# Optimization experiments

Hardware: AMD Instinct MI355X
Metric: run time of the kernel (lower is better)

The kernel has to match this reference:

```python
import math
import jax, jax.numpy as jnp
import numpy as np

B, Q, K, D = 32, 1024, 1024, 128
MASK_VALUE = -1000000.0


def setup_inputs() -> dict:
    key = jax.random.key(0)
    kq, kk, kv, kl = jax.random.split(key, 4)
    return {
        "queries": jax.random.normal(kq, (B, Q, D), dtype=jnp.float32),
        "keys": jax.random.normal(kk, (B, K, D), dtype=jnp.float32),
        "values": jax.random.normal(kv, (B, K, D), dtype=jnp.float32),
        "valid_lens": jax.random.randint(kl, (B,), 1, K + 1, dtype=jnp.int32),
    }


def reference(queries, keys, values, valid_lens):
    d = queries.shape[-1]
    # scores: [B, Q, K]
    scores = jnp.einsum("bqd,bkd->bqk", queries, keys) / math.sqrt(d)
    # key-padding mask: position k valid iff k < valid_lens[b] (broadcast over queries)
    mask = jnp.arange(keys.shape[1])[None, None, :] < valid_lens[:, None, None]
    scores = jnp.where(mask, scores, MASK_VALUE)
    attn = jax.nn.softmax(scores, axis=-1)
    # dropout p=0.0 -> identity
    return jnp.einsum("bqk,bkv->bqv", attn, values)
```

## Files before the change

kernel.cpp:

```cpp
#include <hip/hip_runtime.h>
#include <math.h>

typedef _Float16 f16;
typedef __attribute__((ext_vector_type(8))) _Float16 f16x8;
typedef __attribute__((ext_vector_type(4))) _Float16 f16x4;
typedef __attribute__((ext_vector_type(4))) float f32x4;

constexpr int BATCH = 32;
constexpr int QL = 1024;
constexpr int KL = 1024;
constexpr int D = 128;
constexpr int BQ = 64;
constexpr int BK = 64;
constexpr int DKP = 136;
constexpr int BKP = 72;

#define CSC 0.12752863187087177f

static __device__ __forceinline__ f16x4 pk4(float x, float y, float z, float w) {
  auto a = __builtin_amdgcn_cvt_pkrtz(x, y);
  auto b = __builtin_amdgcn_cvt_pkrtz(z, w);
  f16x4 h;
  h[0] = (f16)a[0]; h[1] = (f16)a[1]; h[2] = (f16)b[0]; h[3] = (f16)b[1];
  return h;
}
static __device__ __forceinline__ f16x8 pk8(float4 u, float4 v) {
  f16x4 a = pk4(u.x, u.y, u.z, u.w);
  f16x4 b = pk4(v.x, v.y, v.z, v.w);
  f16x8 h;
  h[0] = a[0]; h[1] = a[1]; h[2] = a[2]; h[3] = a[3];
  h[4] = b[0]; h[5] = b[1]; h[6] = b[2]; h[7] = b[3];
  return h;
}

template <int CTRL>
static __device__ __forceinline__ float dppf(float v) {
  int x = __float_as_int(v);
  x = __builtin_amdgcn_update_dpp(x, x, CTRL, 0xf, 0xf, false);
  return __int_as_float(x);
}
static __device__ __forceinline__ float rmax16(float v) {
  v = fmaxf(v, dppf<0xB1>(v));
  v = fmaxf(v, dppf<0x4E>(v));
  v = fmaxf(v, dppf<0x141>(v));
  v = fmaxf(v, dppf<0x140>(v));
  return v;
}
static __device__ __forceinline__ float rsum16(float v) {
  v += dppf<0xB1>(v);
  v += dppf<0x4E>(v);
  v += dppf<0x141>(v);
  v += dppf<0x140>(v);
  return v;
}

__global__ __launch_bounds__(256, 2)
void attn_fwd(const float* __restrict__ Qp, const float* __restrict__ Kp,
              const float* __restrict__ Vp, const int* __restrict__ VLp,
              float* __restrict__ Op) {
  __shared__ f16 sK[2][BK][DKP];
  __shared__ f16 sVT[2][D][BKP];
  __shared__ f16 sP[4][16][BKP];
  __shared__ int sN[32];
  __shared__ int sB;

  const int tid  = threadIdx.x;
  const int wave = tid >> 6, lane = tid & 63;
  const int l16  = lane & 15, quad = lane >> 4;

  if (tid < 32) sN[tid] = (VLp[tid] + BK - 1) / BK;
  __syncthreads();
  if (tid < 32) {
    int nb = sN[tid], r = 0;
    #pragma unroll
    for (int k = 0; k < 32; ++k) {
      int nk = sN[k];
      r += (nk > nb) || (nk == nb && k < tid);
    }
    sN[tid] = r;
  }
  __syncthreads();
  const int c = blockIdx.x & 255;
  const int s = (blockIdx.x < 256) ? c : (511 - c);
  if (tid < 32 && sN[tid] == (s >> 4)) sB = tid;
  __syncthreads();
  const int b  = sB;
  const int qt = s & 15;
  const int vl = VLp[b];

  const float* Kb = Kp + (size_t)b * KL * D;
  const float* Vb = Vp + (size_t)b * KL * D;
  const int ntiles = (vl + BK - 1) / BK;

  float4 kreg[8], vreg[8];

  auto issue_loads = [&](int t) {
    const float4* Kt = (const float4*)(Kb + (size_t)t * BK * D);
    #pragma unroll
    for (int i = 0; i < 4; ++i) {
      int cc = tid + i * 256;
      int row = cc >> 4, d04 = (cc & 15) * 2;
      kreg[2 * i]     = Kt[row * 32 + d04];
      kreg[2 * i + 1] = Kt[row * 32 + d04 + 1];
    }
    const float* Vt = Vb + (size_t)t * BK * D;
    #pragma unroll
    for (int i = 0; i < 2; ++i) {
      int f = tid + i * 256;
      const float* base = Vt + (size_t)((f & 15) * 4) * D + (f >> 4) * 4;
      vreg[i * 4 + 0] = *(const float4*)(base);
      vreg[i * 4 + 1] = *(const float4*)(base + D);
      vreg[i * 4 + 2] = *(const float4*)(base + 2 * D);
      vreg[i * 4 + 3] = *(const float4*)(base + 3 * D);
    }
  };
  auto drain = [&](int buf) {
    #pragma unroll
    for (int i = 0; i < 4; ++i) {
      int cc = tid + i * 256;
      int row = cc >> 4, d0 = (cc & 15) * 8;
      int rp = (row & 3) * 16 + (row >> 2);
      *(f16x8*)&sK[buf][rp][d0] = pk8(kreg[2 * i], kreg[2 * i + 1]);
    }
    #pragma unroll
    for (int i = 0; i < 2; ++i) {
      int f = tid + i * 256;
      int k0 = (f & 15) * 4, d0 = (f >> 4) * 4;
      float4 r0 = vreg[i*4+0], r1 = vreg[i*4+1], r2 = vreg[i*4+2], r3 = vreg[i*4+3];
      *(f16x4*)&sVT[buf][d0 + 0][k0] = pk4(r0.x, r1.x, r2.x, r3.x);
      *(f16x4*)&sVT[buf][d0 + 1][k0] = pk4(r0.y, r1.y, r2.y, r3.y);
      *(f16x4*)&sVT[buf][d0 + 2][k0] = pk4(r0.z, r1.z, r2.z, r3.z);
      *(f16x4*)&sVT[buf][d0 + 3][k0] = pk4(r0.w, r1.w, r2.w, r3.w);
    }
  };

  const float* Qb = Qp + ((size_t)(b * QL + qt * BQ + wave * 16 + l16)) * D;
  f16x8 qfrag[4];
  #pragma unroll
  for (int kc = 0; kc < 4; ++kc) {
    const float* p = Qb + kc * 32 + quad * 8;
    qfrag[kc] = pk8(*(const float4*)p, *(const float4*)(p + 4));
  }

  auto s_mfma = [&](int buf, f32x4* out) {
    #pragma unroll
    for (int ct = 0; ct < 4; ++ct) {
      f32x4 cacc = (f32x4){0.f, 0.f, 0.f, 0.f};
      #pragma unroll
      for (int kc = 0; kc < 4; ++kc) {
        f16x8 kf = *(const f16x8*)&sK[buf][ct * 16 + l16][kc * 32 + quad * 8];
        cacc = __builtin_amdgcn_mfma_f32_16x16x32_f16(qfrag[kc], kf, cacc, 0, 0, 0);
      }
      out[ct] = cacc;
    }
  };

  float m2[4]   = {-INFINITY, -INFINITY, -INFINITY, -INFINITY};
  float lsum[4] = {0.f, 0.f, 0.f, 0.f};
  f32x4 o[8];
  #pragma unroll
  for (int dt = 0; dt < 8; ++dt) o[dt] = (f32x4){0.f, 0.f, 0.f, 0.f};

  f32x4 sv[4], svn[4];

  issue_loads(0);
  drain(0);
  if (ntiles > 1) issue_loads(1);
  __syncthreads();
  s_mfma(0, sv);
  if (ntiles > 1) drain(1);
  __syncthreads();

  for (int t = 0; t < ntiles; ++t) {
    const int cur = t & 1, nxt = cur ^ 1;

    if (t + 1 < ntiles) s_mfma(nxt, svn);
    if (t + 2 < ntiles) issue_loads(t + 2);

    #pragma unroll
    for (int ct = 0; ct < 4; ++ct) {
      bool ok = (t * BK + l16 * 4 + ct) < vl;
      #pragma unroll
      for (int r = 0; r < 4; ++r)
        sv[ct][r] = ok ? sv[ct][r] * CSC : -1.0e9f;
    }
    float mnew[4], alpha[4];
    #pragma unroll
    for (int r = 0; r < 4; ++r) {
      float v = fmaxf(fmaxf(sv[0][r], sv[1][r]), fmaxf(sv[2][r], sv[3][r]));
      v = rmax16(v);
      mnew[r]  = fmaxf(m2[r], v);
      alpha[r] = __builtin_amdgcn_exp2f(m2[r] - mnew[r]);
      m2[r]    = mnew[r];
    }
    #pragma unroll
    for (int r = 0; r < 4; ++r) {
      float ls = 0.f;
      #pragma unroll
      for (int ct = 0; ct < 4; ++ct) {
        float p = __builtin_amdgcn_exp2f(sv[ct][r] - mnew[r]);
        sv[ct][r] = p;
        ls += p;
      }
      lsum[r] = lsum[r] * alpha[r] + rsum16(ls);
      *(f16x4*)&sP[wave][quad * 4 + r][l16 * 4] =
          pk4(sv[0][r], sv[1][r], sv[2][r], sv[3][r]);
      #pragma unroll
      for (int dt = 0; dt < 8; ++dt) o[dt][r] *= alpha[r];
    }

    asm volatile("s_waitcnt lgkmcnt(0)" ::: "memory");

    #pragma unroll
    for (int ks = 0; ks < 2; ++ks) {
      f16x8 pf = *(const f16x8*)&sP[wave][l16][ks * 32 + quad * 8];
      #pragma unroll
      for (int dt = 0; dt < 8; ++dt) {
        f16x8 vf = *(const f16x8*)&sVT[cur][dt * 16 + l16][ks * 32 + quad * 8];
        o[dt] = __builtin_amdgcn_mfma_f32_16x16x32_f16(pf, vf, o[dt], 0, 0, 0);
      }
    }

    __syncthreads();
    if (t + 2 < ntiles) drain(cur);
    __syncthreads();

    #pragma unroll
    for (int ct = 0; ct < 4; ++ct) sv[ct] = svn[ct];
  }

  float* Ob = Op + ((size_t)(b * QL + qt * BQ + wave * 16)) * D;
  #pragma unroll
  for (int r = 0; r < 4; ++r) {
    float inv = 1.0f / lsum[r];
    int row = quad * 4 + r;
    #pragma unroll
    for (int dt = 0; dt < 8; ++dt)
      Ob[(size_t)row * D + dt * 16 + l16] = o[dt][r] * inv;
  }
}

extern "C" void kernel_launch(void* const* d_in, const int* in_sizes, int n_in,
                              void* d_out, int out_size, void* d_ws, size_t ws_size,
                              hipStream_t stream) {
  const float* Qp = (const float*)d_in[0];
  const float* Kp = (const float*)d_in[1];
  const float* Vp = (const float*)d_in[2];
  const int*   VL = (const int*)d_in[3];
  float* Op = (float*)d_out;

  attn_fwd<<<dim3(QL / BQ * BATCH), dim3(256), 0, stream>>>(Qp, Kp, Vp, VL, Op);
}
```

Measured before the change: 121.5 us.

## Single-buffer K/V shared tiles and drop QK lookahead to fit three blocks per CU

Shrinks the shared-memory staging from double-buffered to single-buffered K and V^T tiles, and removes the software-pipelined QK^T lookahead (svn) so scores are computed in the same iteration they are used. The launch bound rises from 2 to 3 blocks per CU, aiming for more resident waves to hide latency instead of relying on intra-block pipelining. In exchange, each iteration now serializes the QK MFMA and the PV MFMA behind barriers. It also leaves fewer registers per thread, which risks spills.

```diff
diff --git a/kernel.cpp b/kernel.cpp
--- a/kernel.cpp
+++ b/kernel.cpp
@@ -54,12 +54,12 @@
   return v;
 }
 
-__global__ __launch_bounds__(256, 2)
+__global__ __launch_bounds__(256, 3)
 void attn_fwd(const float* __restrict__ Qp, const float* __restrict__ Kp,
               const float* __restrict__ Vp, const int* __restrict__ VLp,
               float* __restrict__ Op) {
-  __shared__ f16 sK[2][BK][DKP];
-  __shared__ f16 sVT[2][D][BKP];
+  __shared__ f16 sK[BK][DKP];
+  __shared__ f16 sVT[D][BKP];
   __shared__ f16 sP[4][16][BKP];
   __shared__ int sN[32];
   __shared__ int sB;
@@ -114,23 +114,23 @@
       vreg[i * 4 + 3] = *(const float4*)(base + 3 * D);
     }
   };
-  auto drain = [&](int buf) {
+  auto drain = [&]() {
     #pragma unroll
     for (int i = 0; i < 4; ++i) {
       int cc = tid + i * 256;
       int row = cc >> 4, d0 = (cc & 15) * 8;
       int rp = (row & 3) * 16 + (row >> 2);
-      *(f16x8*)&sK[buf][rp][d0] = pk8(kreg[2 * i], kreg[2 * i + 1]);
+      *(f16x8*)&sK[rp][d0] = pk8(kreg[2 * i], kreg[2 * i + 1]);
     }
     #pragma unroll
     for (int i = 0; i < 2; ++i) {
       int f = tid + i * 256;
       int k0 = (f & 15) * 4, d0 = (f >> 4) * 4;
       float4 r0 = vreg[i*4+0], r1 = vreg[i*4+1], r2 = vreg[i*4+2], r3 = vreg[i*4+3];
-      *(f16x4*)&sVT[buf][d0 + 0][k0] = pk4(r0.x, r1.x, r2.x, r3.x);
-      *(f16x4*)&sVT[buf][d0 + 1][k0] = pk4(r0.y, r1.y, r2.y, r3.y);
-      *(f16x4*)&sVT[buf][d0 + 2][k0] = pk4(r0.z, r1.z, r2.z, r3.z);
-      *(f16x4*)&sVT[buf][d0 + 3][k0] = pk4(r0.w, r1.w, r2.w, r3.w);
+      *(f16x4*)&sVT[d0 + 0][k0] = pk4(r0.x, r1.x, r2.x, r3.x);
+      *(f16x4*)&sVT[d0 + 1][k0] = pk4(r0.y, r1.y, r2.y, r3.y);
+      *(f16x4*)&sVT[d0 + 2][k0] = pk4(r0.z, r1.z, r2.z, r3.z);
+      *(f16x4*)&sVT[d0 + 3][k0] = pk4(r0.w, r1.w, r2.w, r3.w);
     }
   };
 
@@ -142,40 +142,32 @@
     qfrag[kc] = pk8(*(const float4*)p, *(const float4*)(p + 4));
   }
 
-  auto s_mfma = [&](int buf, f32x4* out) {
-    #pragma unroll
-    for (int ct = 0; ct < 4; ++ct) {
-      f32x4 cacc = (f32x4){0.f, 0.f, 0.f, 0.f};
-      #pragma unroll
-      for (int kc = 0; kc < 4; ++kc) {
-        f16x8 kf = *(const f16x8*)&sK[buf][ct * 16 + l16][kc * 32 + quad * 8];
-        cacc = __builtin_amdgcn_mfma_f32_16x16x32_f16(qfrag[kc], kf, cacc, 0, 0, 0);
-      }
-      out[ct] = cacc;
-    }
-  };
-
   float m2[4]   = {-INFINITY, -INFINITY, -INFINITY, -INFINITY};
   float lsum[4] = {0.f, 0.f, 0.f, 0.f};
   f32x4 o[8];
   #pragma unroll
   for (int dt = 0; dt < 8; ++dt) o[dt] = (f32x4){0.f, 0.f, 0.f, 0.f};
 
-  f32x4 sv[4], svn[4];
-
   issue_loads(0);
-  drain(0);
-  if (ntiles > 1) issue_loads(1);
-  __syncthreads();
-  s_mfma(0, sv);
-  if (ntiles > 1) drain(1);
+  drain();
   __syncthreads();
 
   for (int t = 0; t < ntiles; ++t) {
-    const int cur = t & 1, nxt = cur ^ 1;
-
-    if (t + 1 < ntiles) s_mfma(nxt, svn);
-    if (t + 2 < ntiles) issue_loads(t + 2);
+    const bool more = (t + 1 < ntiles);
+
+    if (more) issue_loads(t + 1);
+
+    f32x4 sv[4];
+    #pragma unroll
+    for (int ct = 0; ct < 4; ++ct) {
+      f32x4 cacc = (f32x4){0.f, 0.f, 0.f, 0.f};
+      #pragma unroll
+      for (int kc = 0; kc < 4; ++kc) {
+        f16x8 kf = *(const f16x8*)&sK[ct * 16 + l16][kc * 32 + quad * 8];
+        cacc = __builtin_amdgcn_mfma_f32_16x16x32_f16(qfrag[kc], kf, cacc, 0, 0, 0);
+      }
+      sv[ct] = cacc;
+    }
 
     #pragma unroll
     for (int ct = 0; ct < 4; ++ct) {
@@ -184,6 +176,7 @@
       for (int r = 0; r < 4; ++r)
         sv[ct][r] = ok ? sv[ct][r] * CSC : -1.0e9f;
     }
+
     float mnew[4], alpha[4];
     #pragma unroll
     for (int r = 0; r < 4; ++r) {
@@ -216,17 +209,16 @@
       f16x8 pf = *(const f16x8*)&sP[wave][l16][ks * 32 + quad * 8];
       #pragma unroll
       for (int dt = 0; dt < 8; ++dt) {
-        f16x8 vf = *(const f16x8*)&sVT[cur][dt * 16 + l16][ks * 32 + quad * 8];
+        f16x8 vf = *(const f16x8*)&sVT[dt * 16 + l16][ks * 32 + quad * 8];
         o[dt] = __builtin_amdgcn_mfma_f32_16x16x32_f16(pf, vf, o[dt], 0, 0, 0);
       }
     }
 
-    __syncthreads();
-    if (t + 2 < ntiles) drain(cur);
-    __syncthreads();
-
-    #pragma unroll
-    for (int ct = 0; ct < 4; ++ct) sv[ct] = svn[ct];
+    if (more) {
+      __syncthreads();
+      drain();
+      __syncthreads();
+    }
   }
 
   float* Ob = Op + ((size_t)(b * QL + qt * BQ + wave * 16)) * D;
```

New measurement: 137.4 us. 1.13x slower.
